# Optimization experiments

Hardware: AMD Instinct MI355X
Metric: run time of the kernel (lower is better)

## Reference

```python
import jax, jax.numpy as jnp
import numpy as np

B, N, H, OUT, L = 32, 4096, 256, 256, 4
EPS = 1e-5


def _build_edge_index(num_nodes):
    grid = int(np.sqrt(num_nodes)) + 1
    edges = []
    for i in range(num_nodes):
        col = i % grid
        if col < grid - 1 and i + 1 < num_nodes:
            edges.append([i, i + 1]); edges.append([i + 1, i])
        if i + grid < num_nodes:
            edges.append([i, i + grid]); edges.append([i + grid, i])
    return np.asarray(edges, dtype=np.int64).T  # [2, E]


def setup_inputs() -> dict:
    key = jax.random.key(0)
    ks = jax.random.split(key, 12)
    s = 0.02
    x = (jax.random.uniform(ks[0], (B, N)) < 0.1).astype(jnp.float32)  # syndrome bits
    edge_index = jnp.asarray(_build_edge_index(N))
    return {
        "x": x,
        "edge_index": edge_index,
        "proj_w": jax.random.normal(ks[1], (1, H)) * s,
        "proj_b": jnp.zeros((H,)),
        "conv_w": jax.random.normal(ks[2], (L, H, H)) * s,
        "conv_b": jnp.zeros((L, H)),
        "ln_g": jnp.ones((L, H)),
        "ln_b": jnp.zeros((L, H)),
        "h1_w": jax.random.normal(ks[3], (H, H)) * s,
        "h1_b": jnp.zeros((H,)),
        "h2_w": jax.random.normal(ks[4], (H, OUT)) * s,
        "h2_b": jnp.zeros((OUT,)),
    }


def reference(x, edge_index, proj_w, proj_b, conv_w, conv_b, ln_g, ln_b,
              h1_w, h1_b, h2_w, h2_b):
    batch, n = x.shape
    total = batch * n
    # batched edge index: replicate per sample with node offsets
    offsets = (jnp.arange(batch, dtype=edge_index.dtype) * n)
    ei = (edge_index[:, None, :] + offsets[None, :, None]).reshape(2, -1)
    src, dst = ei[0], ei[1]

    h = x.reshape(total, 1) @ proj_w + proj_b  # [total, H]

    # GCN symmetric norm with self-loops (degree = in-degree + 1)
    deg = jnp.zeros((total,), h.dtype).at[dst].add(1.0) + 1.0
    dinv_sqrt = jax.lax.rsqrt(deg)
    enorm = (dinv_sqrt[src] * dinv_sqrt[dst])[:, None]  # [E, 1]
    self_norm = (1.0 / deg)[:, None]                    # [total, 1]

    for l in range(L):
        t = h @ conv_w[l]                                   # transform
        agg = jnp.zeros_like(t).at[dst].add(enorm * t[src])  # scatter-add
        t = agg + self_norm * t + conv_b[l]
        mu = t.mean(-1, keepdims=True)
        var = ((t - mu) ** 2).mean(-1, keepdims=True)
        t = (t - mu) * jax.lax.rsqrt(var + EPS) * ln_g[l] + ln_b[l]
        h = jax.nn.relu(t)

    pooled = h.reshape(batch, n, -1).mean(axis=1)  # global_mean_pool (equal-size graphs)
    return jax.nn.relu(pooled @ h1_w + h1_b) @ h2_w + h2_b
```

## Files before the change

### kernel.cpp

```cpp
#include <hip/hip_runtime.h>
#include <cstdint>
#include <cstddef>

#define TOTAL (32*4096)
#define H 256
#define NLAYER 4

typedef __bf16 bf16x8 __attribute__((ext_vector_type(8)));
typedef float floatx4 __attribute__((ext_vector_type(4)));

__device__ __forceinline__ float u2f(unsigned int i) {
  union { unsigned int u; float f; } p; p.u = i; return p.f;
}
__device__ __forceinline__ float bf2f_lo(unsigned int u) { return u2f(u << 16); }
__device__ __forceinline__ float bf2f_hi(unsigned int u) { return u2f(u & 0xffff0000u); }
__device__ __forceinline__ unsigned int f2bf(float f) {
  union { float f; unsigned int i; } p; p.f = f;
  unsigned int r = p.i + 0x7fffu + ((p.i >> 16) & 1u);
  return r >> 16;
}
__device__ __forceinline__ unsigned int cvt_pk_bf16(float lo, float hi) {
  unsigned int r;
  asm("v_cvt_pk_bf16_f32 %0, %1, %2" : "=v"(r) : "v"(lo), "v"(hi));
  return r;
}

__device__ __forceinline__ float dinv_of(int n) {
  int col = n % 65;
  int deg = 1;
  deg += (n >= 1 && col != 0) ? 1 : 0;
  deg += (col != 64 && n <= 4094) ? 1 : 0;
  deg += (n >= 65) ? 1 : 0;
  deg += (n <= 4030) ? 1 : 0;
  return rsqrtf((float)deg);
}

__device__ __forceinline__ void load8(const unsigned short* p, float* v) {
  uint4 u = *reinterpret_cast<const uint4*>(p);
  v[0] = bf2f_lo(u.x); v[1] = bf2f_hi(u.x);
  v[2] = bf2f_lo(u.y); v[3] = bf2f_hi(u.y);
  v[4] = bf2f_lo(u.z); v[5] = bf2f_hi(u.z);
  v[6] = bf2f_lo(u.w); v[7] = bf2f_hi(u.w);
}
__device__ __forceinline__ uint4 pack8(const float* v) {
  uint4 u;
  u.x = cvt_pk_bf16(v[0], v[1]);
  u.y = cvt_pk_bf16(v[2], v[3]);
  u.z = cvt_pk_bf16(v[4], v[5]);
  u.w = cvt_pk_bf16(v[6], v[7]);
  return u;
}
__device__ __forceinline__ void loadf8(const float* p, float* v) {
  float4 a = *reinterpret_cast<const float4*>(p);
  float4 b = *reinterpret_cast<const float4*>(p + 4);
  v[0] = a.x; v[1] = a.y; v[2] = a.z; v[3] = a.w;
  v[4] = b.x; v[5] = b.y; v[6] = b.z; v[7] = b.w;
}

__global__ void k_transpose(const float* __restrict__ src,
                            unsigned short* __restrict__ wt,
                            float* __restrict__ pooled) {
  int idx = blockIdx.x * 256 + threadIdx.x;
  if (blockIdx.x < 32) pooled[idx] = 0.0f;
  int n = idx & 255;
  int k = (idx >> 8) & 255;
  int l = idx >> 16;
  int wgrp = n >> 6, cc = n & 3, ll = (n >> 2) & 15;
  int ngrp = wgrp * 4 + cc;
  int c = k >> 5, lq = (k >> 3) & 3, j = k & 7;
  wt[(size_t)l * 65536 + (ngrp * 8 + c) * 512 + (lq * 16 + ll) * 8 + j] =
      (unsigned short)f2bf(src[idx]);
}

template <int AGG, int POOL, int GPROJ>
__global__ __launch_bounds__(256, 4)
void k_gemm_ln(const unsigned short* __restrict__ Hin,
               const float* __restrict__ x,
               const float* __restrict__ pw,
               const float* __restrict__ pb,
               const unsigned short* __restrict__ Bf,
               const float* __restrict__ cb,
               const float* __restrict__ lg,
               const float* __restrict__ lb,
               unsigned short* __restrict__ Hout,
               float* __restrict__ pooled) {
  __shared__ alignas(16) unsigned char smem_u[64 * 130 * 4];
  unsigned short* As = reinterpret_cast<unsigned short*>(smem_u);
  float*          p2 = reinterpret_cast<float*>(smem_u);
  __shared__ float red2[4][64][2];
  __shared__ float musr[64][2];
  const int t = threadIdx.x;
  const int w = t >> 6, lane = t & 63;
  const int lq = lane >> 4, ll = lane & 15;
  const int tile = (blockIdx.x & 7) * (gridDim.x >> 3) + (blockIdx.x >> 3);
  const int m0 = tile * 64;
  const int wc = w * 64;
  const int ar = t >> 2;
  const int ak = (t & 3) * 8;

  {
    const int gi = m0 + ar;
    const int nd = gi & 4095;
    const int col = nd % 65;
    const float di = dinv_of(nd);
    if (GPROJ) {
      const int base = gi - nd;
      float sx = di * x[gi];
      float sc = di;
      if (nd >= 1 && col != 0)     { float dj = dinv_of(nd - 1);  sx += dj * x[base + nd - 1];  sc += dj; }
      if (col != 64 && nd <= 4094) { float dj = dinv_of(nd + 1);  sx += dj * x[base + nd + 1];  sc += dj; }
      if (nd >= 65)                { float dj = dinv_of(nd - 65); sx += dj * x[base + nd - 65]; sc += dj; }
      if (nd <= 4030)              { float dj = dinv_of(nd + 65); sx += dj * x[base + nd + 65]; sc += dj; }
      sx *= di; sc *= di;
#pragma unroll
      for (int c = 0; c < 8; c++) {
        const int k0 = c * 32 + ak;
        float wv[8], bv[8], o[8];
        loadf8(pw + k0, wv);
        loadf8(pb + k0, bv);
#pragma unroll
        for (int q = 0; q < 8; q++) o[q] = sx * wv[q] + sc * bv[q];
        *reinterpret_cast<uint4*>(&As[c * 2048 + ar * 32 + ak]) = pack8(o);
      }
    } else if (AGG) {
      int j1 = gi, j2 = gi, j3 = gi, j4 = gi;
      float w1 = 0.f, w2 = 0.f, w3 = 0.f, w4 = 0.f;
      if (nd >= 1 && col != 0)     { j1 = gi - 1;  w1 = dinv_of(nd - 1); }
      if (col != 64 && nd <= 4094) { j2 = gi + 1;  w2 = dinv_of(nd + 1); }
      if (nd >= 65)                { j3 = gi - 65; w3 = dinv_of(nd - 65); }
      if (nd <= 4030)              { j4 = gi + 65; w4 = dinv_of(nd + 65); }
      const unsigned short* r0p = Hin + (size_t)gi * 256 + ak;
      const unsigned short* r1p = Hin + (size_t)j1 * 256 + ak;
      const unsigned short* r2p = Hin + (size_t)j2 * 256 + ak;
      const unsigned short* r3p = Hin + (size_t)j3 * 256 + ak;
      const unsigned short* r4p = Hin + (size_t)j4 * 256 + ak;
#pragma unroll
      for (int c = 0; c < 8; c++) {
        const int k0 = c * 32;
        float a0[8], a1[8], a2[8], a3[8], a4[8];
        load8(r0p + k0, a0);
        load8(r1p + k0, a1);
        load8(r2p + k0, a2);
        load8(r3p + k0, a3);
        load8(r4p + k0, a4);
        float o[8];
#pragma unroll
        for (int q = 0; q < 8; q++)
          o[q] = di * (di * a0[q] + w1 * a1[q] + w2 * a2[q] + w3 * a3[q] + w4 * a4[q]);
        *reinterpret_cast<uint4*>(&As[c * 2048 + ar * 32 + ak]) = pack8(o);
      }
    } else {
      const unsigned short* r0p = Hin + (size_t)gi * 256 + ak;
#pragma unroll
      for (int c = 0; c < 8; c++)
        *reinterpret_cast<uint4*>(&As[c * 2048 + ar * 32 + ak]) =
            *reinterpret_cast<const uint4*>(r0p + c * 32);
    }
  }
  __syncthreads();

  floatx4 acc[4][4] = {};
  const unsigned short* bbase = Bf + (size_t)(w * 4) * 8 * 512 + lane * 8;

#pragma unroll
  for (int c = 0; c < 8; c++) {
    bf16x8 bfr[4], af[4];
#pragma unroll
    for (int cc = 0; cc < 4; cc++)
      bfr[cc] = *reinterpret_cast<const bf16x8*>(bbase + (cc * 8 + c) * 512);
#pragma unroll
    for (int r = 0; r < 4; r++)
      af[r] = *reinterpret_cast<const bf16x8*>(&As[c * 2048 + (r * 16 + ll) * 32 + lq * 8]);
#pragma unroll
    for (int r = 0; r < 4; r++)
#pragma unroll
      for (int cc = 0; cc < 4; cc++)
        acc[r][cc] = __builtin_amdgcn_mfma_f32_16x16x32_bf16(af[r], bfr[cc], acc[r][cc], 0, 0, 0);
  }

  const int colbase = wc + (ll << 2);
  const float4 cb4 = *reinterpret_cast<const float4*>(cb + colbase);
  const float4 lg4 = *reinterpret_cast<const float4*>(lg + colbase);
  const float4 lb4 = *reinterpret_cast<const float4*>(lb + colbase);
  const float cbv[4]  = {cb4.x, cb4.y, cb4.z, cb4.w};
  const float gamv[4] = {lg4.x, lg4.y, lg4.z, lg4.w};
  const float betv[4] = {lb4.x, lb4.y, lb4.z, lb4.w};

  __syncthreads();
  {
    const int slice2 = (w * 16 + ll) * 2;
#pragma unroll
    for (int r = 0; r < 4; r++) {
#pragma unroll
      for (int reg = 0; reg < 4; reg++) {
        float sv = 0.f, sq = 0.f;
#pragma unroll
        for (int c = 0; c < 4; c++) {
          float v = acc[r][c][reg] + cbv[c];
          sv += v; sq += v * v;
        }
        const int row = r * 16 + lq * 4 + reg;
        *reinterpret_cast<float2*>(&p2[row * 130 + slice2]) = make_float2(sv, sq);
      }
    }
  }
  __syncthreads();
  {
    const int row = t & 63, qu = t >> 6;
    float s = 0.f, q = 0.f;
#pragma unroll
    for (int i = 0; i < 16; i++) {
      float2 pq = *reinterpret_cast<const float2*>(&p2[row * 130 + (qu * 16 + i) * 2]);
      s += pq.x; q += pq.y;
    }
    red2[qu][row][0] = s;
    red2[qu][row][1] = q;
  }
  __syncthreads();
  if (t < 64) {
    float s = red2[0][t][0] + red2[1][t][0] + red2[2][t][0] + red2[3][t][0];
    float q = red2[0][t][1] + red2[1][t][1] + red2[2][t][1] + red2[3][t][1];
    float mu = s * (1.0f / 256.0f);
    float var = fmaxf(q * (1.0f / 256.0f) - mu * mu, 0.0f);
    musr[t][0] = mu;
    musr[t][1] = rsqrtf(var + 1e-5f);
  }
  __syncthreads();

  if (POOL == 0) {
#pragma unroll
    for (int r = 0; r < 4; r++) {
#pragma unroll
      for (int reg = 0; reg < 4; reg++) {
        int row = r * 16 + lq * 4 + reg;
        float mu = musr[row][0], rs = musr[row][1];
        float hv[4];
#pragma unroll
        for (int c = 0; c < 4; c++) {
          float v = (acc[r][c][reg] + cbv[c] - mu) * rs * gamv[c] + betv[c];
          hv[c] = fmaxf(v, 0.0f);
        }
        uint2 st;
        st.x = cvt_pk_bf16(hv[0], hv[1]);
        st.y = cvt_pk_bf16(hv[2], hv[3]);
        *reinterpret_cast<uint2*>(&Hout[(size_t)(m0 + row) * 256 + colbase]) = st;
      }
    }
  } else {
    float csum[4] = {0.f, 0.f, 0.f, 0.f};
#pragma unroll
    for (int r = 0; r < 4; r++) {
#pragma unroll
      for (int reg = 0; reg < 4; reg++) {
        int row = r * 16 + lq * 4 + reg;
        float mu = musr[row][0], rs = musr[row][1];
#pragma unroll
        for (int c = 0; c < 4; c++) {
          float hv = (acc[r][c][reg] + cbv[c] - mu) * rs * gamv[c] + betv[c];
          csum[c] += fmaxf(hv, 0.0f);
        }
      }
    }
#pragma unroll
    for (int c = 0; c < 4; c++) {
      csum[c] += __shfl_xor(csum[c], 16, 64);
      csum[c] += __shfl_xor(csum[c], 32, 64);
    }
    if (lq == 0) {
      int b = m0 >> 12;
#pragma unroll
      for (int c = 0; c < 4; c++)
        atomicAdd(&pooled[b * 256 + colbase + c], csum[c] * (1.0f / 4096.0f));
    }
  }
}

__global__ void k_head(const float* __restrict__ pooled,
                       const float* __restrict__ w1,
                       const float* __restrict__ b1,
                       const float* __restrict__ w2,
                       const float* __restrict__ b2,
                       float* __restrict__ out) {
  const int b = blockIdx.x;
  const int t = threadIdx.x;
  __shared__ float row[256];
  __shared__ float y1[256];
  row[t] = pooled[b * 256 + t];
  __syncthreads();
  float s = b1[t];
#pragma unroll 8
  for (int k = 0; k < 256; k++) s += row[k] * w1[k * 256 + t];
  y1[t] = fmaxf(s, 0.0f);
  __syncthreads();
  float s2 = b2[t];
#pragma unroll 8
  for (int k = 0; k < 256; k++) s2 += y1[k] * w2[k * 256 + t];
  out[b * 256 + t] = s2;
}

extern "C" void kernel_launch(void* const* d_in, const int* in_sizes, int n_in,
                              void* d_out, int out_size, void* d_ws, size_t ws_size,
                              hipStream_t stream) {
  (void)in_sizes; (void)n_in; (void)out_size; (void)ws_size;
  const float* x      = (const float*)d_in[0];
  const float* proj_w = (const float*)d_in[2];
  const float* proj_b = (const float*)d_in[3];
  const float* conv_w = (const float*)d_in[4];
  const float* conv_b = (const float*)d_in[5];
  const float* ln_g   = (const float*)d_in[6];
  const float* ln_b   = (const float*)d_in[7];
  const float* h1_w   = (const float*)d_in[8];
  const float* h1_b   = (const float*)d_in[9];
  const float* h2_w   = (const float*)d_in[10];
  const float* h2_b   = (const float*)d_in[11];

  char* ws = (char*)d_ws;
  const size_t act_bytes = (size_t)TOTAL * H * 2;
  unsigned short* ha     = (unsigned short*)ws;
  unsigned short* hb     = (unsigned short*)(ws + act_bytes);
  unsigned short* wt     = (unsigned short*)(ws + 2 * act_bytes);
  float*          pooled = (float*)(ws + 2 * act_bytes + (size_t)NLAYER * H * H * 2);

  k_transpose<<<NLAYER * H * H / 256, 256, 0, stream>>>(conv_w, wt, pooled);

  const int GB = TOTAL / 64;
  k_gemm_ln<0, 0, 1><<<GB, 256, 0, stream>>>(nullptr, x, proj_w, proj_b,
      wt + 0 * (size_t)H * H, conv_b + 0 * H, ln_g + 0 * H, ln_b + 0 * H, hb, nullptr);
  k_gemm_ln<1, 0, 0><<<GB, 256, 0, stream>>>(hb, nullptr, nullptr, nullptr,
      wt + 1 * (size_t)H * H, conv_b + 1 * H, ln_g + 1 * H, ln_b + 1 * H, ha, nullptr);
  k_gemm_ln<1, 0, 0><<<GB, 256, 0, stream>>>(ha, nullptr, nullptr, nullptr,
      wt + 2 * (size_t)H * H, conv_b + 2 * H, ln_g + 2 * H, ln_b + 2 * H, hb, nullptr);
  k_gemm_ln<1, 1, 0><<<GB, 256, 0, stream>>>(hb, nullptr, nullptr, nullptr,
      wt + 3 * (size_t)H * H, conv_b + 3 * H, ln_g + 3 * H, ln_b + 3 * H, nullptr, pooled);

  k_head<<<32, 256, 0, stream>>>(pooled, h1_w, h1_b, h2_w, h2_b, (float*)d_out);
}
```

Measured before the change: 273.8 us.

## Switch activations and weights to fp16 with pre-scaled rows and packed-half aggregation

Converts activations, weights and MFMA from bf16 to fp16, and stores each layer's output pre-multiplied by its node's dinv. The next layer's neighbor aggregation then becomes masked packed-half additions plus one scale, with no per-element bf16-to-float unpacking or dinv recomputation per neighbor. This cuts ALU work in the gather stage. In exchange, fp16 has a narrower range and accumulates the 5-term sum in half precision, which adds rounding error.

```diff
diff --git a/kernel.cpp b/kernel.cpp
--- a/kernel.cpp
+++ b/kernel.cpp
@@ -6,24 +6,9 @@
 #define H 256
 #define NLAYER 4
 
-typedef __bf16 bf16x8 __attribute__((ext_vector_type(8)));
+typedef _Float16 f16x8 __attribute__((ext_vector_type(8)));
+typedef _Float16 f16x4 __attribute__((ext_vector_type(4)));
 typedef float floatx4 __attribute__((ext_vector_type(4)));
-
-__device__ __forceinline__ float u2f(unsigned int i) {
-  union { unsigned int u; float f; } p; p.u = i; return p.f;
-}
-__device__ __forceinline__ float bf2f_lo(unsigned int u) { return u2f(u << 16); }
-__device__ __forceinline__ float bf2f_hi(unsigned int u) { return u2f(u & 0xffff0000u); }
-__device__ __forceinline__ unsigned int f2bf(float f) {
-  union { float f; unsigned int i; } p; p.f = f;
-  unsigned int r = p.i + 0x7fffu + ((p.i >> 16) & 1u);
-  return r >> 16;
-}
-__device__ __forceinline__ unsigned int cvt_pk_bf16(float lo, float hi) {
-  unsigned int r;
-  asm("v_cvt_pk_bf16_f32 %0, %1, %2" : "=v"(r) : "v"(lo), "v"(hi));
-  return r;
-}
 
 __device__ __forceinline__ float dinv_of(int n) {
   int col = n % 65;
@@ -35,21 +20,6 @@
   return rsqrtf((float)deg);
 }
 
-__device__ __forceinline__ void load8(const unsigned short* p, float* v) {
-  uint4 u = *reinterpret_cast<const uint4*>(p);
-  v[0] = bf2f_lo(u.x); v[1] = bf2f_hi(u.x);
-  v[2] = bf2f_lo(u.y); v[3] = bf2f_hi(u.y);
-  v[4] = bf2f_lo(u.z); v[5] = bf2f_hi(u.z);
-  v[6] = bf2f_lo(u.w); v[7] = bf2f_hi(u.w);
-}
-__device__ __forceinline__ uint4 pack8(const float* v) {
-  uint4 u;
-  u.x = cvt_pk_bf16(v[0], v[1]);
-  u.y = cvt_pk_bf16(v[2], v[3]);
-  u.z = cvt_pk_bf16(v[4], v[5]);
-  u.w = cvt_pk_bf16(v[6], v[7]);
-  return u;
-}
 __device__ __forceinline__ void loadf8(const float* p, float* v) {
   float4 a = *reinterpret_cast<const float4*>(p);
   float4 b = *reinterpret_cast<const float4*>(p + 4);
@@ -68,27 +38,28 @@
   int wgrp = n >> 6, cc = n & 3, ll = (n >> 2) & 15;
   int ngrp = wgrp * 4 + cc;
   int c = k >> 5, lq = (k >> 3) & 3, j = k & 7;
-  wt[(size_t)l * 65536 + (ngrp * 8 + c) * 512 + (lq * 16 + ll) * 8 + j] =
-      (unsigned short)f2bf(src[idx]);
+  _Float16 hv = (_Float16)src[idx];
+  union { _Float16 h; unsigned short u; } pk; pk.h = hv;
+  wt[(size_t)l * 65536 + (ngrp * 8 + c) * 512 + (lq * 16 + ll) * 8 + j] = pk.u;
 }
 
 template <int AGG, int POOL, int GPROJ>
 __global__ __launch_bounds__(256, 4)
-void k_gemm_ln(const unsigned short* __restrict__ Hin,
+void k_gemm_ln(const _Float16* __restrict__ Hin,
                const float* __restrict__ x,
                const float* __restrict__ pw,
                const float* __restrict__ pb,
-               const unsigned short* __restrict__ Bf,
+               const _Float16* __restrict__ Bf,
                const float* __restrict__ cb,
                const float* __restrict__ lg,
                const float* __restrict__ lb,
-               unsigned short* __restrict__ Hout,
+               _Float16* __restrict__ Hout,
                float* __restrict__ pooled) {
   __shared__ alignas(16) unsigned char smem_u[64 * 130 * 4];
-  unsigned short* As = reinterpret_cast<unsigned short*>(smem_u);
-  float*          p2 = reinterpret_cast<float*>(smem_u);
+  _Float16* As = reinterpret_cast<_Float16*>(smem_u);
+  float*    p2 = reinterpret_cast<float*>(smem_u);
   __shared__ float red2[4][64][2];
-  __shared__ float musr[64][2];
+  __shared__ float musr[64][4];
   const int t = threadIdx.x;
   const int w = t >> 6, lane = t & 63;
   const int lq = lane >> 4, ll = lane & 15;
@@ -115,67 +86,65 @@
 #pragma unroll
       for (int c = 0; c < 8; c++) {
         const int k0 = c * 32 + ak;
-        float wv[8], bv[8], o[8];
+        float wv[8], bv[8];
         loadf8(pw + k0, wv);
         loadf8(pb + k0, bv);
-#pragma unroll
-        for (int q = 0; q < 8; q++) o[q] = sx * wv[q] + sc * bv[q];
-        *reinterpret_cast<uint4*>(&As[c * 2048 + ar * 32 + ak]) = pack8(o);
+        f16x8 oh;
+#pragma unroll
+        for (int q = 0; q < 8; q++) oh[q] = (_Float16)(sx * wv[q] + sc * bv[q]);
+        *reinterpret_cast<f16x8*>(&As[c * 2048 + ar * 32 + ak]) = oh;
       }
     } else if (AGG) {
       int j1 = gi, j2 = gi, j3 = gi, j4 = gi;
-      float w1 = 0.f, w2 = 0.f, w3 = 0.f, w4 = 0.f;
-      if (nd >= 1 && col != 0)     { j1 = gi - 1;  w1 = dinv_of(nd - 1); }
-      if (col != 64 && nd <= 4094) { j2 = gi + 1;  w2 = dinv_of(nd + 1); }
-      if (nd >= 65)                { j3 = gi - 65; w3 = dinv_of(nd - 65); }
-      if (nd <= 4030)              { j4 = gi + 65; w4 = dinv_of(nd + 65); }
-      const unsigned short* r0p = Hin + (size_t)gi * 256 + ak;
-      const unsigned short* r1p = Hin + (size_t)j1 * 256 + ak;
-      const unsigned short* r2p = Hin + (size_t)j2 * 256 + ak;
-      const unsigned short* r3p = Hin + (size_t)j3 * 256 + ak;
-      const unsigned short* r4p = Hin + (size_t)j4 * 256 + ak;
+      _Float16 m1 = (_Float16)0.f, m2 = (_Float16)0.f, m3 = (_Float16)0.f, m4 = (_Float16)0.f;
+      if (nd >= 1 && col != 0)     { j1 = gi - 1;  m1 = (_Float16)1.f; }
+      if (col != 64 && nd <= 4094) { j2 = gi + 1;  m2 = (_Float16)1.f; }
+      if (nd >= 65)                { j3 = gi - 65; m3 = (_Float16)1.f; }
+      if (nd <= 4030)              { j4 = gi + 65; m4 = (_Float16)1.f; }
+      const _Float16 dih = (_Float16)di;
+      const _Float16* r0p = Hin + (size_t)gi * 256 + ak;
+      const _Float16* r1p = Hin + (size_t)j1 * 256 + ak;
+      const _Float16* r2p = Hin + (size_t)j2 * 256 + ak;
+      const _Float16* r3p = Hin + (size_t)j3 * 256 + ak;
+      const _Float16* r4p = Hin + (size_t)j4 * 256 + ak;
 #pragma unroll
       for (int c = 0; c < 8; c++) {
         const int k0 = c * 32;
-        float a0[8], a1[8], a2[8], a3[8], a4[8];
-        load8(r0p + k0, a0);
-        load8(r1p + k0, a1);
-        load8(r2p + k0, a2);
-        load8(r3p + k0, a3);
-        load8(r4p + k0, a4);
-        float o[8];
-#pragma unroll
-        for (int q = 0; q < 8; q++)
-          o[q] = di * (di * a0[q] + w1 * a1[q] + w2 * a2[q] + w3 * a3[q] + w4 * a4[q]);
-        *reinterpret_cast<uint4*>(&As[c * 2048 + ar * 32 + ak]) = pack8(o);
+        f16x8 a0 = *reinterpret_cast<const f16x8*>(r0p + k0);
+        f16x8 a1 = *reinterpret_cast<const f16x8*>(r1p + k0);
+        f16x8 a2 = *reinterpret_cast<const f16x8*>(r2p + k0);
+        f16x8 a3 = *reinterpret_cast<const f16x8*>(r3p + k0);
+        f16x8 a4 = *reinterpret_cast<const f16x8*>(r4p + k0);
+        f16x8 o = (a0 + a1 * m1 + a2 * m2 + a3 * m3 + a4 * m4) * dih;
+        *reinterpret_cast<f16x8*>(&As[c * 2048 + ar * 32 + ak]) = o;
       }
     } else {
-      const unsigned short* r0p = Hin + (size_t)gi * 256 + ak;
+      const _Float16* r0p = Hin + (size_t)gi * 256 + ak;
 #pragma unroll
       for (int c = 0; c < 8; c++)
-        *reinterpret_cast<uint4*>(&As[c * 2048 + ar * 32 + ak]) =
-            *reinterpret_cast<const uint4*>(r0p + c * 32);
+        *reinterpret_cast<f16x8*>(&As[c * 2048 + ar * 32 + ak]) =
+            *reinterpret_cast<const f16x8*>(r0p + c * 32);
     }
   }
   __syncthreads();
 
   floatx4 acc[4][4] = {};
-  const unsigned short* bbase = Bf + (size_t)(w * 4) * 8 * 512 + lane * 8;
+  const _Float16* bbase = Bf + (size_t)(w * 4) * 8 * 512 + lane * 8;
 
 #pragma unroll
   for (int c = 0; c < 8; c++) {
-    bf16x8 bfr[4], af[4];
+    f16x8 bfr[4], af[4];
 #pragma unroll
     for (int cc = 0; cc < 4; cc++)
-      bfr[cc] = *reinterpret_cast<const bf16x8*>(bbase + (cc * 8 + c) * 512);
+      bfr[cc] = *reinterpret_cast<const f16x8*>(bbase + (cc * 8 + c) * 512);
 #pragma unroll
     for (int r = 0; r < 4; r++)
-      af[r] = *reinterpret_cast<const bf16x8*>(&As[c * 2048 + (r * 16 + ll) * 32 + lq * 8]);
+      af[r] = *reinterpret_cast<const f16x8*>(&As[c * 2048 + (r * 16 + ll) * 32 + lq * 8]);
 #pragma unroll
     for (int r = 0; r < 4; r++)
 #pragma unroll
       for (int cc = 0; cc < 4; cc++)
-        acc[r][cc] = __builtin_amdgcn_mfma_f32_16x16x32_bf16(af[r], bfr[cc], acc[r][cc], 0, 0, 0);
+        acc[r][cc] = __builtin_amdgcn_mfma_f32_16x16x32_f16(af[r], bfr[cc], acc[r][cc], 0, 0, 0);
   }
 
   const int colbase = wc + (ll << 2);
@@ -224,6 +193,7 @@
     float var = fmaxf(q * (1.0f / 256.0f) - mu * mu, 0.0f);
     musr[t][0] = mu;
     musr[t][1] = rsqrtf(var + 1e-5f);
+    musr[t][2] = dinv_of((m0 + t) & 4095);
   }
   __syncthreads();
 
@@ -233,17 +203,14 @@
 #pragma unroll
       for (int reg = 0; reg < 4; reg++) {
         int row = r * 16 + lq * 4 + reg;
-        float mu = musr[row][0], rs = musr[row][1];
-        float hv[4];
+        float mu = musr[row][0], rs = musr[row][1], dr = musr[row][2];
+        f16x4 st;
 #pragma unroll
         for (int c = 0; c < 4; c++) {
           float v = (acc[r][c][reg] + cbv[c] - mu) * rs * gamv[c] + betv[c];
-          hv[c] = fmaxf(v, 0.0f);
+          st[c] = (_Float16)(fmaxf(v, 0.0f) * dr);
         }
-        uint2 st;
-        st.x = cvt_pk_bf16(hv[0], hv[1]);
-        st.y = cvt_pk_bf16(hv[2], hv[3]);
-        *reinterpret_cast<uint2*>(&Hout[(size_t)(m0 + row) * 256 + colbase]) = st;
+        *reinterpret_cast<f16x4*>(&Hout[(size_t)(m0 + row) * 256 + colbase]) = st;
       }
     }
   } else {
@@ -316,12 +283,13 @@
 
   char* ws = (char*)d_ws;
   const size_t act_bytes = (size_t)TOTAL * H * 2;
-  unsigned short* ha     = (unsigned short*)ws;
-  unsigned short* hb     = (unsigned short*)(ws + act_bytes);
-  unsigned short* wt     = (unsigned short*)(ws + 2 * act_bytes);
-  float*          pooled = (float*)(ws + 2 * act_bytes + (size_t)NLAYER * H * H * 2);
-
-  k_transpose<<<NLAYER * H * H / 256, 256, 0, stream>>>(conv_w, wt, pooled);
+  _Float16* ha     = (_Float16*)ws;
+  _Float16* hb     = (_Float16*)(ws + act_bytes);
+  unsigned short* wt_u = (unsigned short*)(ws + 2 * act_bytes);
+  _Float16* wt     = (_Float16*)wt_u;
+  float*    pooled = (float*)(ws + 2 * act_bytes + (size_t)NLAYER * H * H * 2);
+
+  k_transpose<<<NLAYER * H * H / 256, 256, 0, stream>>>(conv_w, wt_u, pooled);
 
   const int GB = TOTAL / 64;
   k_gemm_ln<0, 0, 1><<<GB, 256, 0, stream>>>(nullptr, x, proj_w, proj_b,
```

New measurement: 273.5 us. Within noise of the previous version (-0.1%).
